# Performance work log

Measured on AMD Instinct MI355X. Metric: run time of the kernel, lower is better.

## Reference

```python
import jax, jax.numpy as jnp
import numpy as np

D_MODEL = 256
N_HEADS = 8
N_LEVELS = 3
N_POINTS = 4
HEAD_DIM = D_MODEL // N_HEADS
SPATIAL_SHAPES = [(80, 80), (40, 40), (20, 20)]
B = 16
LEN_Q = 300
N_TOTAL = sum(h * w for h, w in SPATIAL_SHAPES)  # 8400
N_LP = N_LEVELS * N_POINTS


def setup_inputs() -> dict:
    key = jax.random.key(0)
    ks = jax.random.split(key, 8)
    s = 0.02
    return {
        "query": jax.random.normal(ks[0], (B, LEN_Q, D_MODEL), jnp.float32),
        "reference_points": jax.random.uniform(ks[1], (B, LEN_Q, N_LEVELS, 2), jnp.float32),
        "input_flatten": jax.random.normal(ks[2], (B, N_TOTAL, D_MODEL), jnp.float32),
        "W_off": jax.random.normal(ks[3], (D_MODEL, N_HEADS * N_LP * 2), jnp.float32) * s,
        "b_off": jnp.zeros((N_HEADS * N_LP * 2,), jnp.float32),
        "W_attn": jax.random.normal(ks[4], (D_MODEL, N_HEADS * N_LP), jnp.float32) * s,
        "b_attn": jnp.zeros((N_HEADS * N_LP,), jnp.float32),
        "W_val": jax.random.normal(ks[5], (D_MODEL, D_MODEL), jnp.float32) * s,
        "b_val": jnp.zeros((D_MODEL,), jnp.float32),
        "W_out": jax.random.normal(ks[6], (D_MODEL, D_MODEL), jnp.float32) * s,
        "b_out": jnp.zeros((D_MODEL,), jnp.float32),
    }


def _ms_deform_core(value, sampling_locations, attention_weights):
    # value: (B, n_heads, head_dim, N_total); locations: (B, Lq, H, L, P, 2) in [0,1]
    Bq, Lq = sampling_locations.shape[0], sampling_locations.shape[1]
    BN = Bq * N_HEADS
    grids = 2.0 * sampling_locations - 1.0
    starts = np.cumsum([0] + [h * w for h, w in SPATIAL_SHAPES])
    sampled_levels = []
    for lid, (H, W) in enumerate(SPATIAL_SHAPES):
        val_l = value[..., starts[lid]:starts[lid + 1]]                    # (B,H,hd,HW)
        val_flat = val_l.reshape(BN, HEAD_DIM, H * W).transpose(0, 2, 1)   # (BN,HW,hd)
        g = grids[:, :, :, lid].transpose(0, 2, 1, 3, 4).reshape(BN, Lq, N_POINTS, 2)
        ix = ((g[..., 0] + 1.0) * W - 1.0) / 2.0
        iy = ((g[..., 1] + 1.0) * H - 1.0) / 2.0
        ix0 = jnp.floor(ix).astype(jnp.int32)
        iy0 = jnp.floor(iy).astype(jnp.int32)
        ix1 = ix0 + 1
        iy1 = iy0 + 1
        fx = (ix - ix0.astype(ix.dtype))[..., None]
        fy = (iy - iy0.astype(iy.dtype))[..., None]

        def corner(iyc, ixc):
            valid = ((ixc >= 0) & (ixc < W) & (iyc >= 0) & (iyc < H)).astype(val_flat.dtype)
            idx = (jnp.clip(iyc, 0, H - 1) * W + jnp.clip(ixc, 0, W - 1))
            idx = idx.reshape(BN, Lq * N_POINTS, 1)
            v = jnp.take_along_axis(val_flat, idx, axis=1)
            return v.reshape(BN, Lq, N_POINTS, HEAD_DIM) * valid[..., None]

        v00 = corner(iy0, ix0)
        v01 = corner(iy0, ix1)
        v10 = corner(iy1, ix0)
        v11 = corner(iy1, ix1)
        sampled = ((1 - fx) * (1 - fy)) * v00 + (fx * (1 - fy)) * v01 \
                + ((1 - fx) * fy) * v10 + (fx * fy) * v11
        sampled_levels.append(sampled.transpose(0, 3, 1, 2))               # (BN,hd,Lq,P)
    sv = jnp.stack(sampled_levels, axis=-2).reshape(BN, HEAD_DIM, Lq, N_LP)
    a = attention_weights.transpose(0, 2, 1, 3).reshape(BN, 1, Lq, N_LP)
    out = jnp.sum(sv * a, axis=-1)                                         # (BN,hd,Lq)
    return out.reshape(Bq, D_MODEL, Lq).transpose(0, 2, 1)                 # (B,Lq,D)


def reference(query, reference_points, input_flatten,
              W_off, b_off, W_attn, b_attn, W_val, b_val, W_out, b_out):
    Bq, Lq = query.shape[0], query.shape[1]
    value = input_flatten @ W_val + b_val
    value = value.reshape(Bq, -1, N_HEADS, HEAD_DIM).transpose(0, 2, 3, 1)  # (B,H,hd,N)
    off = (query @ W_off + b_off).reshape(Bq, Lq, N_HEADS, N_LEVELS, N_POINTS, 2)
    attn = jax.nn.softmax((query @ W_attn + b_attn).reshape(Bq, Lq, N_HEADS, N_LP), axis=-1)
    # offset normalizer is (W,H) per level (x first)
    norm = jnp.array([[w, h] for h, w in SPATIAL_SHAPES], jnp.float32)
    loc = reference_points[:, :, None, :, None, :] + off / norm[None, None, None, :, None, :]
    out = _ms_deform_core(value, loc, attn)
    return out @ W_out + b_out
```

## Files before the change

### kernel.cpp

```cpp
#include <hip/hip_runtime.h>
#include <hip/hip_bf16.h>

#define DM 256
#define NH 8
#define HD 32
#define NLV 3
#define NPT 4
#define NLP 12
#define BB 16
#define LQ 300
#define NT 8400
#define MROWS (BB * NT)
#define QROWS (BB * LQ)
#define KP3 264
#define VB (MROWS / 64)

typedef __bf16 bf16x8 __attribute__((ext_vector_type(8)));
typedef float  f32x16 __attribute__((ext_vector_type(16)));

#define GPTR(x) ((const __attribute__((address_space(1))) unsigned int*)(x))
#define LPTR(x) ((__attribute__((address_space(3))) unsigned int*)(x))

__global__ void k_wt(const float* __restrict__ W_val,
                     const float* __restrict__ W_off,
                     const float* __restrict__ W_attn,
                     const float* __restrict__ W_out,
                     __hip_bfloat16* __restrict__ Wf,
                     __hip_bfloat16* __restrict__ Wf2,
                     __hip_bfloat16* __restrict__ Wf3)
{
    const int n = blockIdx.x;
    const int k = threadIdx.x;
    if (n < 256) {
        Wf[(size_t)(k >> 3) * 2048 + n * 8 + (k & 7)] =
            __float2bfloat16(W_val[(size_t)k * 256 + n]);
    } else if (n < 544) {
        const int n2 = n - 256;
        float v = (n2 < 192) ? W_off[(size_t)k * 192 + n2]
                             : W_attn[(size_t)k * 96 + (n2 - 192)];
        Wf2[(size_t)(k >> 3) * 2304 + n2 * 8 + (k & 7)] = __float2bfloat16(v);
    } else {
        const int n3 = n - 544;
        Wf3[(size_t)(k >> 3) * 2048 + n3 * 8 + (k & 7)] =
            __float2bfloat16(W_out[(size_t)k * 256 + n3]);
    }
}

__global__ __launch_bounds__(256) void k_mm1(
    const float* __restrict__ A,
    const __hip_bfloat16* __restrict__ Wf,
    const float* __restrict__ bval,
    __hip_bfloat16* __restrict__ V,
    const float* __restrict__ Q,
    const __hip_bfloat16* __restrict__ Wf2,
    const float* __restrict__ boff,
    const float* __restrict__ battn,
    float* __restrict__ off_out,
    float* __restrict__ attn_out)
{
    __shared__ __align__(16) float Asf[8192];

    const int t    = threadIdx.x;
    const int wave = t >> 6;
    const int lane = t & 63;
    const int lm   = lane & 31;
    const int kh   = lane >> 5;

    if (blockIdx.x < VB) {
        const int m0 = blockIdx.x * 64;

        f32x16 acc[2][2];
#pragma unroll
        for (int i = 0; i < 2; i++)
#pragma unroll
            for (int j = 0; j < 2; j++)
#pragma unroll
                for (int e = 0; e < 16; e++) acc[i][j][e] = 0.f;

        const __hip_bfloat16* wf0 = Wf + (size_t)(wave * 64 + lm) * 8 + kh * 2048;
        const int sw = lm & 15;

#pragma unroll
        for (int p = 0; p < 4; ++p) {
            const int row = p * 16 + (t >> 4);
            const int sc  = (t & 15) ^ (row & 15);
            const float* gsrc = A + (size_t)(m0 + row) * 256 + sc * 4;
            __builtin_amdgcn_global_load_lds(GPTR(gsrc),
                LPTR((char*)Asf + p * 4096 + (t & 192) * 16), 16, 0, 0);
        }
        __syncthreads();

#pragma unroll
        for (int it = 0; it < 4; ++it) {
            float* cur = Asf + (it & 1) * 4096;
            if (it < 3) {
                float* nxt = Asf + ((it & 1) ^ 1) * 4096;
#pragma unroll
                for (int p = 0; p < 4; ++p) {
                    const int row = p * 16 + (t >> 4);
                    const int sc  = (t & 15) ^ (row & 15);
                    const float* gsrc = A + (size_t)(m0 + row) * 256 + (it + 1) * 64 + sc * 4;
                    __builtin_amdgcn_global_load_lds(GPTR(gsrc),
                        LPTR((char*)nxt + p * 4096 + (t & 192) * 16), 16, 0, 0);
                }
            }
#pragma unroll
            for (int g4 = 0; g4 < 4; ++g4) {
                const int g  = it * 4 + g4;
                const int s0 = g4 * 4 + kh * 2;
                float4 x0 = *(const float4*)(cur + lm * 64 + (((s0)     ^ sw) << 2));
                float4 x1 = *(const float4*)(cur + lm * 64 + (((s0 + 1) ^ sw) << 2));
                float4 y0 = *(const float4*)(cur + (32 + lm) * 64 + (((s0)     ^ sw) << 2));
                float4 y1 = *(const float4*)(cur + (32 + lm) * 64 + (((s0 + 1) ^ sw) << 2));
                union { __hip_bfloat162 h2[4]; bf16x8 v; } u0, u1;
                u0.h2[0] = __float22bfloat162_rn(make_float2(x0.x, x0.y));
                u0.h2[1] = __float22bfloat162_rn(make_float2(x0.z, x0.w));
                u0.h2[2] = __float22bfloat162_rn(make_float2(x1.x, x1.y));
                u0.h2[3] = __float22bfloat162_rn(make_float2(x1.z, x1.w));
                u1.h2[0] = __float22bfloat162_rn(make_float2(y0.x, y0.y));
                u1.h2[1] = __float22bfloat162_rn(make_float2(y0.z, y0.w));
                u1.h2[2] = __float22bfloat162_rn(make_float2(y1.x, y1.y));
                u1.h2[3] = __float22bfloat162_rn(make_float2(y1.z, y1.w));
                bf16x8 b0 = *(const bf16x8*)(wf0 + (size_t)g * 4096);
                bf16x8 b1 = *(const bf16x8*)(wf0 + (size_t)g * 4096 + 256);
                acc[0][0] = __builtin_amdgcn_mfma_f32_32x32x16_bf16(u0.v, b0, acc[0][0], 0, 0, 0);
                acc[0][1] = __builtin_amdgcn_mfma_f32_32x32x16_bf16(u0.v, b1, acc[0][1], 0, 0, 0);
                acc[1][0] = __builtin_amdgcn_mfma_f32_32x32x16_bf16(u1.v, b0, acc[1][0], 0, 0, 0);
                acc[1][1] = __builtin_amdgcn_mfma_f32_32x32x16_bf16(u1.v, b1, acc[1][1], 0, 0, 0);
            }
            if (it < 3) __syncthreads();
        }

        const int bb  = m0 / NT;
        const int bnd = (bb + 1) * NT;
#pragma unroll
        for (int i = 0; i < 2; i++) {
#pragma unroll
            for (int j = 0; j < 2; j++) {
                const int n  = wave * 64 + j * 32 + lm;
                const float bn = bval[n];
                const int h  = n >> 5;
                const int d  = n & 31;
#pragma unroll
                for (int r2 = 0; r2 < 16; r2++) {
                    int rl = (r2 & 3) + 8 * (r2 >> 2) + 4 * kh;
                    int m  = m0 + i * 32 + rl;
                    int b  = bb + ((m >= bnd) ? 1 : 0);
                    int pos = m - b * NT;
                    V[((size_t)(b * NH + h) * NT + pos) * HD + d] =
                        __float2bfloat16(acc[i][j][r2] + bn);
                }
            }
        }
    } else {
        const int m0 = (blockIdx.x - VB) * 32;

        f32x16 acc[3];
#pragma unroll
        for (int j = 0; j < 3; j++)
#pragma unroll
            for (int e = 0; e < 16; e++) acc[j][e] = 0.f;

        const __hip_bfloat16* wf0 = Wf2 + (size_t)(wave * 96 + lm) * 8 + kh * 2304;
        const int sw = lm & 15;

#pragma unroll
        for (int p = 0; p < 2; ++p) {
            const int row = p * 16 + (t >> 4);
            const int sc  = (t & 15) ^ (row & 15);
            const float* gsrc = Q + (size_t)(m0 + row) * 256 + sc * 4;
            __builtin_amdgcn_global_load_lds(GPTR(gsrc),
                LPTR((char*)Asf + p * 4096 + (t & 192) * 16), 16, 0, 0);
        }
        __syncthreads();

#pragma unroll
        for (int it = 0; it < 4; ++it) {
            float* cur = Asf + (it & 1) * 2048;
            if (it < 3) {
                float* nxt = Asf + ((it & 1) ^ 1) * 2048;
#pragma unroll
                for (int p = 0; p < 2; ++p) {
                    const int row = p * 16 + (t >> 4);
                    const int sc  = (t & 15) ^ (row & 15);
                    const float* gsrc = Q + (size_t)(m0 + row) * 256 + (it + 1) * 64 + sc * 4;
                    __builtin_amdgcn_global_load_lds(GPTR(gsrc),
                        LPTR((char*)nxt + p * 4096 + (t & 192) * 16), 16, 0, 0);
                }
            }
            if (wave < 3) {
#pragma unroll
                for (int g4 = 0; g4 < 4; ++g4) {
                    const int g  = it * 4 + g4;
                    const int s0 = g4 * 4 + kh * 2;
                    float4 x0 = *(const float4*)(cur + lm * 64 + (((s0)     ^ sw) << 2));
                    float4 x1 = *(const float4*)(cur + lm * 64 + (((s0 + 1) ^ sw) << 2));
                    union { __hip_bfloat162 h2[4]; bf16x8 v; } ua;
                    ua.h2[0] = __float22bfloat162_rn(make_float2(x0.x, x0.y));
                    ua.h2[1] = __float22bfloat162_rn(make_float2(x0.z, x0.w));
                    ua.h2[2] = __float22bfloat162_rn(make_float2(x1.x, x1.y));
                    ua.h2[3] = __float22bfloat162_rn(make_float2(x1.z, x1.w));
#pragma unroll
                    for (int j = 0; j < 3; j++) {
                        bf16x8 bf = *(const bf16x8*)(wf0 + (size_t)g * 4608 + j * 256);
                        acc[j] = __builtin_amdgcn_mfma_f32_32x32x16_bf16(ua.v, bf, acc[j], 0, 0, 0);
                    }
                }
            }
            if (it < 3) __syncthreads();
        }

        if (wave < 3) {
#pragma unroll
            for (int j = 0; j < 3; j++) {
                const int n = wave * 96 + j * 32 + lm;
                const float bias_ = (n < 192) ? boff[n] : battn[n - 192];
#pragma unroll
                for (int r2 = 0; r2 < 16; r2++) {
                    int rl = (r2 & 3) + 8 * (r2 >> 2) + 4 * kh;
                    int m  = m0 + rl;
                    float v = acc[j][r2] + bias_;
                    if (n < 192) off_out[(size_t)m * 192 + n] = v;
                    else         attn_out[(size_t)m * 96 + (n - 192)] = v;
                }
            }
        }
    }
}

__global__ __launch_bounds__(256) void k_sample(
    const float* __restrict__ off_raw,
    const float* __restrict__ attn_raw,
    const float* __restrict__ refp,
    const __hip_bfloat16* __restrict__ V,
    __hip_bfloat16* __restrict__ sampled)
{
    const int t = threadIdx.x;

    const int bid  = blockIdx.x;
    const int xcd  = bid & 7;
    const int slot = bid >> 3;
    const int hi   = (slot >= 75) ? 1 : 0;
    const int b    = xcd + (hi << 3);
    const int q0   = (slot - hi * 75) * 4;
    const int bq0  = b * LQ + q0;

    __shared__ float aw[4][96];
    __shared__ float wc[4][96][4];
    __shared__ int   ic[4][96][4];

    if (t < 32) {
        const int q = t >> 3, h = t & 7;
        const float* arp = attn_raw + (size_t)(bq0 + q) * 96 + h * 12;
        float4 x0 = *(const float4*)arp;
        float4 x1 = *(const float4*)(arp + 4);
        float4 x2 = *(const float4*)(arp + 8);
        float v[12] = {x0.x, x0.y, x0.z, x0.w,
                       x1.x, x1.y, x1.z, x1.w,
                       x2.x, x2.y, x2.z, x2.w};
        float mx = -1e30f;
#pragma unroll
        for (int i = 0; i < 12; i++) mx = fmaxf(mx, v[i]);
        float s = 0.f;
#pragma unroll
        for (int i = 0; i < 12; i++) { v[i] = expf(v[i] - mx); s += v[i]; }
        float inv = 1.f / s;
#pragma unroll
        for (int i = 0; i < 12; i++) aw[q][h * 12 + i] = v[i] * inv;
    }
    __syncthreads();

#pragma unroll
    for (int i = t; i < 384; i += 256) {
        const int q  = i / 96;
        const int s  = i - q * 96;
        const int bq = bq0 + q;
        const float dims[3]  = {80.f, 40.f, 20.f};
        const int startsl[3] = {0, 6400, 8000};
        const int idiml[3]   = {80, 40, 20};
        int h = s / 12, lp = s - h * 12, l = lp >> 2, p = lp & 3;
        float2 o2 = *(const float2*)(off_raw + (size_t)bq * 192 + ((h * 3 + l) * 4 + p) * 2);
        float2 r2 = *(const float2*)(refp + (size_t)bq * 6 + l * 2);
        float D  = dims[l];
        float ix = (r2.x + o2.x / D) * D - 0.5f;
        float iy = (r2.y + o2.y / D) * D - 0.5f;
        const int Dl = idiml[l];
        const int st = startsl[l];

        float fix = floorf(ix), fiy = floorf(iy);
        int ix0 = (int)fix, iy0 = (int)fiy;
        int ix1 = ix0 + 1, iy1 = iy0 + 1;
        float fx = ix - fix, fy = iy - fiy;

        float mx0 = (ix0 >= 0 && ix0 < Dl) ? 1.f : 0.f;
        float mx1 = (ix1 >= 0 && ix1 < Dl) ? 1.f : 0.f;
        float my0 = (iy0 >= 0 && iy0 < Dl) ? 1.f : 0.f;
        float my1 = (iy1 >= 0 && iy1 < Dl) ? 1.f : 0.f;

        int cx0 = min(max(ix0, 0), Dl - 1);
        int cx1 = min(max(ix1, 0), Dl - 1);
        int cy0 = min(max(iy0, 0), Dl - 1);
        int cy1 = min(max(iy1, 0), Dl - 1);

        float a = aw[q][s];
        wc[q][s][0] = (1.f - fx) * (1.f - fy) * mx0 * my0 * a;
        wc[q][s][1] = fx * (1.f - fy) * mx1 * my0 * a;
        wc[q][s][2] = (1.f - fx) * fy * mx0 * my1 * a;
        wc[q][s][3] = fx * fy * mx1 * my1 * a;
        ic[q][s][0] = (st + cy0 * Dl + cx0) * HD;
        ic[q][s][1] = (st + cy0 * Dl + cx1) * HD;
        ic[q][s][2] = (st + cy1 * Dl + cx0) * HD;
        ic[q][s][3] = (st + cy1 * Dl + cx1) * HD;
    }
    __syncthreads();

    const int q  = t >> 6;
    const int u  = t & 63;
    const int h  = u >> 3;
    const int dt = (u & 7) * 4;
    const int bq = bq0 + q;
    const __hip_bfloat16* vb = V + (size_t)(b * NH + h) * NT * HD + dt;

    float a0 = 0.f, a1 = 0.f, a2 = 0.f, a3 = 0.f;
#pragma unroll
    for (int lp = 0; lp < 12; lp++) {
        const int s = h * 12 + lp;
        float4 w4 = *(const float4*)(&wc[q][s][0]);
        int4   i4 = *(const int4*)(&ic[q][s][0]);
        union { uint2 u2; __hip_bfloat162 h2[2]; } c0, c1, c2, c3;
        c0.u2 = *(const uint2*)(vb + i4.x);
        c1.u2 = *(const uint2*)(vb + i4.y);
        c2.u2 = *(const uint2*)(vb + i4.z);
        c3.u2 = *(const uint2*)(vb + i4.w);
        float2 f0a = __bfloat1622float2(c0.h2[0]), f0b = __bfloat1622float2(c0.h2[1]);
        float2 f1a = __bfloat1622float2(c1.h2[0]), f1b = __bfloat1622float2(c1.h2[1]);
        float2 f2a = __bfloat1622float2(c2.h2[0]), f2b = __bfloat1622float2(c2.h2[1]);
        float2 f3a = __bfloat1622float2(c3.h2[0]), f3b = __bfloat1622float2(c3.h2[1]);
        a0 = fmaf(w4.x, f0a.x, fmaf(w4.y, f1a.x, fmaf(w4.z, f2a.x, fmaf(w4.w, f3a.x, a0))));
        a1 = fmaf(w4.x, f0a.y, fmaf(w4.y, f1a.y, fmaf(w4.z, f2a.y, fmaf(w4.w, f3a.y, a1))));
        a2 = fmaf(w4.x, f0b.x, fmaf(w4.y, f1b.x, fmaf(w4.z, f2b.x, fmaf(w4.w, f3b.x, a2))));
        a3 = fmaf(w4.x, f0b.y, fmaf(w4.y, f1b.y, fmaf(w4.z, f2b.y, fmaf(w4.w, f3b.y, a3))));
    }
    union { ushort4 s4; __hip_bfloat162 h2[2]; } ou;
    ou.h2[0] = __float22bfloat162_rn(make_float2(a0, a1));
    ou.h2[1] = __float22bfloat162_rn(make_float2(a2, a3));
    *(ushort4*)(sampled + (size_t)bq * 256 + h * 32 + dt) = ou.s4;
}

__global__ __launch_bounds__(256) void k_outproj(
    const __hip_bfloat16* __restrict__ A,
    const __hip_bfloat16* __restrict__ Wf3,
    const float* __restrict__ bias,
    float* __restrict__ out)
{
    __shared__ __hip_bfloat16 As[32 * KP3];

    const int t    = threadIdx.x;
    const int m0   = blockIdx.x * 32;
    const int wave = t >> 6;
    const int lane = t & 63;
    const int lm   = lane & 31;
    const int kh   = lane >> 5;
    const int lk   = kh * 8;
    const int ar   = t >> 3;
    const int ak   = (t & 7) * 8;

    const __hip_bfloat16* apg = A + (size_t)(m0 + ar) * 256 + ak;
    bf16x8 rr[4];
#pragma unroll
    for (int it = 0; it < 4; ++it)
        rr[it] = *(const bf16x8*)(apg + it * 64);
#pragma unroll
    for (int it = 0; it < 4; ++it)
        *(bf16x8*)(&As[ar * KP3 + it * 64 + ak]) = rr[it];
    __syncthreads();

    f32x16 acc[2];
#pragma unroll
    for (int j = 0; j < 2; j++)
#pragma unroll
        for (int e = 0; e < 16; e++) acc[j][e] = 0.f;

    const __hip_bfloat16* wf0 = Wf3 + (size_t)(wave * 64 + lm) * 8 + kh * 2048;

#pragma unroll
    for (int ks = 0; ks < 16; ++ks) {
        bf16x8 af = *(const bf16x8*)(&As[lm * KP3 + ks * 16 + lk]);
        bf16x8 b0 = *(const bf16x8*)(wf0 + (size_t)ks * 4096);
        bf16x8 b1 = *(const bf16x8*)(wf0 + (size_t)ks * 4096 + 256);
        acc[0] = __builtin_amdgcn_mfma_f32_32x32x16_bf16(af, b0, acc[0], 0, 0, 0);
        acc[1] = __builtin_amdgcn_mfma_f32_32x32x16_bf16(af, b1, acc[1], 0, 0, 0);
    }

#pragma unroll
    for (int j = 0; j < 2; j++) {
        const int n = wave * 64 + j * 32 + lm;
        const float bn = bias[n];
#pragma unroll
        for (int r2 = 0; r2 < 16; r2++) {
            int rl = (r2 & 3) + 8 * (r2 >> 2) + 4 * kh;
            int m  = m0 + rl;
            out[(size_t)m * 256 + n] = acc[j][r2] + bn;
        }
    }
}

extern "C" void kernel_launch(void* const* d_in, const int* in_sizes, int n_in,
                              void* d_out, int out_size, void* d_ws, size_t ws_size,
                              hipStream_t stream) {
    const float* query  = (const float*)d_in[0];
    const float* refp   = (const float*)d_in[1];
    const float* inputf = (const float*)d_in[2];
    const float* W_off  = (const float*)d_in[3];
    const float* b_off  = (const float*)d_in[4];
    const float* W_attn = (const float*)d_in[5];
    const float* b_attn = (const float*)d_in[6];
    const float* W_val  = (const float*)d_in[7];
    const float* b_val  = (const float*)d_in[8];
    const float* W_out  = (const float*)d_in[9];
    const float* b_out  = (const float*)d_in[10];
    float* out = (float*)d_out;

    char* ws = (char*)d_ws;
    __hip_bfloat16* value   = (__hip_bfloat16*)ws;
    float* off_raw          = (float*)(ws + 68812800);
    float* attn_raw         = (float*)(ws + 72499200);
    __hip_bfloat16* sampled = (__hip_bfloat16*)(ws + 74342400);
    __hip_bfloat16* Wf      = (__hip_bfloat16*)(ws + 76800000);
    __hip_bfloat16* Wf2     = (__hip_bfloat16*)(ws + 76931072);
    __hip_bfloat16* Wf3     = (__hip_bfloat16*)(ws + 77078528);

    k_wt<<<800, 256, 0, stream>>>(W_val, W_off, W_attn, W_out, Wf, Wf2, Wf3);
    k_mm1<<<VB + QROWS / 32, 256, 0, stream>>>(
        inputf, Wf, b_val, value, query, Wf2, b_off, b_attn, off_raw, attn_raw);
    k_sample<<<1200, 256, 0, stream>>>(off_raw, attn_raw, refp, value, sampled);
    k_outproj<<<QROWS / 32, 256, 0, stream>>>(sampled, Wf3, b_out, out);
}
```

Before: 262.3 us.

## Widen sampling gathers to 16-byte loads and split points across lane pairs

In the deformable sampling kernel, each lane now loads 8 bf16 channels per corner with 16-byte loads instead of 4 channels with 8-byte loads. The 12 level-points of a head are split between two paired lanes, and their partial sums are combined with a lane shuffle. Gathers are issued in explicit double-buffered batches so more loads are in flight before they are consumed. The aim is fewer, wider memory transactions and better latency hiding, at the cost of more registers, a shuffle reduction, and half the lanes idle during the store.

```diff
diff --git a/kernel.cpp b/kernel.cpp
--- a/kernel.cpp
+++ b/kernel.cpp
@@ -228,6 +228,29 @@
     }
 }
 
+#define GATHER4(D0, D1, D2, D3, IV)                    \
+    D0 = *(const uint4*)(vb + (IV).x);                 \
+    D1 = *(const uint4*)(vb + (IV).y);                 \
+    D2 = *(const uint4*)(vb + (IV).z);                 \
+    D3 = *(const uint4*)(vb + (IV).w);
+
+#define CONSUME4(C0, C1, C2, C3, W)                                          \
+    {                                                                        \
+        union { uint4 v; __hip_bfloat162 h2[4]; } q0_, q1_, q2_, q3_;        \
+        q0_.v = C0; q1_.v = C1; q2_.v = C2; q3_.v = C3;                      \
+        _Pragma("unroll")                                                    \
+        for (int k_ = 0; k_ < 4; ++k_) {                                     \
+            float2 p0 = __bfloat1622float2(q0_.h2[k_]);                      \
+            float2 p1 = __bfloat1622float2(q1_.h2[k_]);                      \
+            float2 p2 = __bfloat1622float2(q2_.h2[k_]);                      \
+            float2 p3 = __bfloat1622float2(q3_.h2[k_]);                      \
+            aa[2*k_]   = fmaf((W).x, p0.x, fmaf((W).y, p1.x,                 \
+                         fmaf((W).z, p2.x, fmaf((W).w, p3.x, aa[2*k_]))));   \
+            aa[2*k_+1] = fmaf((W).x, p0.y, fmaf((W).y, p1.y,                 \
+                         fmaf((W).z, p2.y, fmaf((W).w, p3.y, aa[2*k_+1])))); \
+        }                                                                    \
+    }
+
 __global__ __launch_bounds__(256) void k_sample(
     const float* __restrict__ off_raw,
     const float* __restrict__ attn_raw,
@@ -314,37 +337,55 @@
     }
     __syncthreads();
 
-    const int q  = t >> 6;
-    const int u  = t & 63;
-    const int h  = u >> 3;
-    const int dt = (u & 7) * 4;
-    const int bq = bq0 + q;
+    const int q   = t >> 6;
+    const int u   = t & 63;
+    const int h   = u >> 3;
+    const int dg  = (u >> 1) & 3;
+    const int par = u & 1;
+    const int dt  = dg * 8;
+    const int bq  = bq0 + q;
     const __hip_bfloat16* vb = V + (size_t)(b * NH + h) * NT * HD + dt;
 
-    float a0 = 0.f, a1 = 0.f, a2 = 0.f, a3 = 0.f;
-#pragma unroll
-    for (int lp = 0; lp < 12; lp++) {
-        const int s = h * 12 + lp;
-        float4 w4 = *(const float4*)(&wc[q][s][0]);
-        int4   i4 = *(const int4*)(&ic[q][s][0]);
-        union { uint2 u2; __hip_bfloat162 h2[2]; } c0, c1, c2, c3;
-        c0.u2 = *(const uint2*)(vb + i4.x);
-        c1.u2 = *(const uint2*)(vb + i4.y);
-        c2.u2 = *(const uint2*)(vb + i4.z);
-        c3.u2 = *(const uint2*)(vb + i4.w);
-        float2 f0a = __bfloat1622float2(c0.h2[0]), f0b = __bfloat1622float2(c0.h2[1]);
-        float2 f1a = __bfloat1622float2(c1.h2[0]), f1b = __bfloat1622float2(c1.h2[1]);
-        float2 f2a = __bfloat1622float2(c2.h2[0]), f2b = __bfloat1622float2(c2.h2[1]);
-        float2 f3a = __bfloat1622float2(c3.h2[0]), f3b = __bfloat1622float2(c3.h2[1]);
-        a0 = fmaf(w4.x, f0a.x, fmaf(w4.y, f1a.x, fmaf(w4.z, f2a.x, fmaf(w4.w, f3a.x, a0))));
-        a1 = fmaf(w4.x, f0a.y, fmaf(w4.y, f1a.y, fmaf(w4.z, f2a.y, fmaf(w4.w, f3a.y, a1))));
-        a2 = fmaf(w4.x, f0b.x, fmaf(w4.y, f1b.x, fmaf(w4.z, f2b.x, fmaf(w4.w, f3b.x, a2))));
-        a3 = fmaf(w4.x, f0b.y, fmaf(w4.y, f1b.y, fmaf(w4.z, f2b.y, fmaf(w4.w, f3b.y, a3))));
-    }
-    union { ushort4 s4; __hip_bfloat162 h2[2]; } ou;
-    ou.h2[0] = __float22bfloat162_rn(make_float2(a0, a1));
-    ou.h2[1] = __float22bfloat162_rn(make_float2(a2, a3));
-    *(ushort4*)(sampled + (size_t)bq * 256 + h * 32 + dt) = ou.s4;
+    float4 wv[6];
+    int4   iv[6];
+#pragma unroll
+    for (int g = 0; g < 6; ++g) {
+        const int s = h * 12 + g * 2 + par;
+        wv[g] = *(const float4*)(&wc[q][s][0]);
+        iv[g] = *(const int4*)(&ic[q][s][0]);
+    }
+
+    float aa[8];
+#pragma unroll
+    for (int k = 0; k < 8; ++k) aa[k] = 0.f;
+
+    uint4 A0, A1, A2, A3, A4, A5, A6, A7;
+    uint4 B0, B1, B2, B3, B4, B5, B6, B7;
+
+    GATHER4(A0, A1, A2, A3, iv[0]);
+    GATHER4(A4, A5, A6, A7, iv[1]);
+    GATHER4(B0, B1, B2, B3, iv[2]);
+    GATHER4(B4, B5, B6, B7, iv[3]);
+    CONSUME4(A0, A1, A2, A3, wv[0]);
+    CONSUME4(A4, A5, A6, A7, wv[1]);
+    GATHER4(A0, A1, A2, A3, iv[4]);
+    GATHER4(A4, A5, A6, A7, iv[5]);
+    CONSUME4(B0, B1, B2, B3, wv[2]);
+    CONSUME4(B4, B5, B6, B7, wv[3]);
+    CONSUME4(A0, A1, A2, A3, wv[4]);
+    CONSUME4(A4, A5, A6, A7, wv[5]);
+
+#pragma unroll
+    for (int k = 0; k < 8; ++k) aa[k] += __shfl_xor(aa[k], 1, 64);
+
+    if (par == 0) {
+        union { uint4 v; __hip_bfloat162 h2[4]; } ou;
+        ou.h2[0] = __float22bfloat162_rn(make_float2(aa[0], aa[1]));
+        ou.h2[1] = __float22bfloat162_rn(make_float2(aa[2], aa[3]));
+        ou.h2[2] = __float22bfloat162_rn(make_float2(aa[4], aa[5]));
+        ou.h2[3] = __float22bfloat162_rn(make_float2(aa[6], aa[7]));
+        *(uint4*)(sampled + (size_t)bq * 256 + h * 32 + dt) = ou.v;
+    }
 }
 
 __global__ __launch_bounds__(256) void k_outproj(
```

Result: no change. 263.7 us (+0.5%).
